# Optimization experiments

Measured on AMD Instinct MI355X. Metric: run time of the kernel, lower is better.

## Reference

```python
import jax, jax.numpy as jnp
import numpy as np

N = 50000
E = 800000
NFEAT, NHID, NCLASS = 128, 64, 16


def _spmm(row, col, w, x):
    # out[i] = sum_{e: row[e]==i} w[e] * x[col[e]]  -- sparse adj @ x
    return jax.ops.segment_sum(x[col] * w[:, None], row, num_segments=N)


def _gcn_layer(x, row, col, w, W, b):
    return _spmm(row, col, w, x @ W) + b


def setup_inputs() -> dict:
    key = jax.random.key(0)
    ks = jax.random.split(key, 16)
    glorot = lambda k, fi, fo: jax.random.uniform(k, (fi, fo), jnp.float32, -1.0, 1.0) / jnp.sqrt(fi)
    inp = {
        "x": jax.random.normal(ks[0], (N, NFEAT), jnp.float32),
        "edge_row": jax.random.randint(ks[1], (E,), 0, N, jnp.int32),
        "edge_col": jax.random.randint(ks[2], (E,), 0, N, jnp.int32),
        "edge_weight": jax.random.uniform(ks[3], (E,), jnp.float32),
        "W1": glorot(ks[4], NFEAT, NHID), "b1": jnp.zeros((NHID,), jnp.float32),
        "W2": glorot(ks[5], NHID, NHID), "b2": jnp.zeros((NHID,), jnp.float32),
        "W3": glorot(ks[6], NHID, NHID), "b3": jnp.zeros((NHID,), jnp.float32),
        "W4": glorot(ks[7], NHID, NHID), "b4": jnp.zeros((NHID,), jnp.float32),
        "W5": glorot(ks[8], NHID, NCLASS), "b5": jnp.zeros((NCLASS,), jnp.float32),
    }
    return inp


def reference(x, edge_row, edge_col, edge_weight, W1, b1, W2, b2, W3, b3, W4, b4, W5, b5):
    # Inference mode: dropout is identity.
    e1 = _gcn_layer(x, edge_row, edge_col, edge_weight, W1, b1)
    h = jax.nn.relu(e1)
    e2 = _gcn_layer(h, edge_row, edge_col, edge_weight, W2, b2)
    h = jax.nn.relu(e2)
    e3 = _gcn_layer(h, edge_row, edge_col, edge_weight, W3, b3)
    h = jax.nn.relu(e3)
    e4 = _gcn_layer(h, edge_row, edge_col, edge_weight, W4, b4)
    h = jax.nn.relu(e4)
    e5 = _gcn_layer(h, edge_row, edge_col, edge_weight, W5, b5)
    return (jax.nn.log_softmax(e5, axis=1), e1, e2, e3, e4, e5)
```

## Files before the change

kernel.cpp:

```cpp
#include <hip/hip_runtime.h>
#include <math.h>

#define NN 50000
#define NE 800000
#define NFEAT 128
#define NHID 64
#define NCLASS 16
#define NB_SCAN ((NN + 255) / 256)
#define GB ((NN + 63) / 64)
#define SGRP 4
#define ROWS_PER_SGRP ((NN + SGRP - 1) / SGRP)
#define SCHUNKS 392

__device__ inline unsigned short f2bf(float f) {
    unsigned u = __builtin_bit_cast(unsigned, f);
    u += 0x7fffu + ((u >> 16) & 1u);
    return (unsigned short)(u >> 16);
}
__device__ inline float bf2f(unsigned short h) {
    return __builtin_bit_cast(float, (unsigned)h << 16);
}
__device__ inline float pk_w(unsigned v) { return bf2f((unsigned short)(v >> 16)); }
__device__ inline int pk_c(unsigned v) { return (int)(v & 0xffffu); }


__global__ __launch_bounds__(256) void hist_rank_kernel(const int* __restrict__ erow,
                                                        int* __restrict__ deg,
                                                        unsigned* __restrict__ rr, int E) {
    int e = blockIdx.x * 256 + threadIdx.x;
    if (e < E) {
        int r = erow[e];
        int k = atomicAdd(&deg[r], 1);
        rr[e] = ((unsigned)r << 16) | (unsigned)k;
    }
}

__global__ __launch_bounds__(256) void scan_sum_kernel(const int* __restrict__ deg,
                                                       int* __restrict__ blocksum, int n) {
    __shared__ int s[256];
    const int t = threadIdx.x;
    int i = blockIdx.x * 256 + t;
    s[t] = (i < n) ? deg[i] : 0;
    __syncthreads();
#pragma unroll
    for (int off = 128; off > 0; off >>= 1) {
        if (t < off) s[t] += s[t + off];
        __syncthreads();
    }
    if (t == 0) blocksum[blockIdx.x] = s[0];
}

__global__ __launch_bounds__(256) void scan_final_kernel(const int* __restrict__ deg,
                                                         const int* __restrict__ blocksum,
                                                         int* __restrict__ row_ptr, int n) {
    __shared__ int bs[256];
    __shared__ int s[256];
    const int t = threadIdx.x;
    bs[t] = (t < NB_SCAN) ? blocksum[t] : 0;
    __syncthreads();
    for (int off = 1; off < 256; off <<= 1) {
        int u = (t >= off) ? bs[t - off] : 0;
        __syncthreads();
        bs[t] += u;
        __syncthreads();
    }
    const int blockpre = (blockIdx.x == 0) ? 0 : bs[blockIdx.x - 1];

    int i = blockIdx.x * 256 + t;
    int d = (i < n) ? deg[i] : 0;
    s[t] = d;
    __syncthreads();
    for (int off = 1; off < 256; off <<= 1) {
        int u = (t >= off) ? s[t - off] : 0;
        __syncthreads();
        s[t] += u;
        __syncthreads();
    }
    int excl = blockpre + s[t] - d;
    if (i < n) {
        row_ptr[i] = excl;
        if (i == n - 1) row_ptr[n] = excl + d;
    }
}

__global__ __launch_bounds__(256) void scatter_rank_kernel(const unsigned* __restrict__ rr,
                                                           const int* __restrict__ ecol,
                                                           const float* __restrict__ ew,
                                                           const int* __restrict__ row_ptr,
                                                           unsigned* __restrict__ pk, int E) {
    const int g = blockIdx.x & (SGRP - 1);
    const int chunk = blockIdx.x / SGRP;
    const int CH = (E + SCHUNKS - 1) / SCHUNKS;
    const int lo = chunk * CH;
    const int hi = (lo + CH < E) ? lo + CH : E;
    for (int e = lo + threadIdx.x; e < hi; e += 256) {
        unsigned v = rr[e];
        int r = (int)(v >> 16);
        if (r / ROWS_PER_SGRP == g) {
            int pos = row_ptr[r] + (int)(v & 0xffffu);
            pk[pos] = ((unsigned)f2bf(ew[e]) << 16) | (unsigned)ecol[e];
        }
    }
}

template <int K, bool RELU_IN>
__global__ __launch_bounds__(256) void gemm64_kernel(const float* __restrict__ in,
                                                     const float* __restrict__ Wg,
                                                     unsigned short* __restrict__ outb, int M) {
    constexpr int KC = 64;
    __shared__ float xs[KC][68];
    __shared__ float Ws[KC][64];
    const int t = threadIdx.x;
    const int tx = t % 16;
    const int ty = t / 16;
    const int r0 = blockIdx.x * 64;

    float acc[4][4];
#pragma unroll
    for (int i = 0; i < 4; i++)
#pragma unroll
        for (int j = 0; j < 4; j++) acc[i][j] = 0.f;

    for (int k0 = 0; k0 < K; k0 += KC) {
        for (int i = t * 4; i < KC * 64; i += 1024) {
            *(float4*)&Ws[i / 64][i % 64] = *(const float4*)&Wg[(size_t)k0 * 64 + i];
        }
        {
            const int r = t / 4;
            const int q = t % 4;
            const int gr = r0 + r;
#pragma unroll
            for (int i = 0; i < 4; i++) {
                int k = q * 16 + i * 4;
                float4 v;
                if (gr < M)
                    v = *(const float4*)&in[(size_t)gr * K + k0 + k];
                else
                    v = make_float4(0.f, 0.f, 0.f, 0.f);
                if (RELU_IN) {
                    v.x = fmaxf(v.x, 0.f);
                    v.y = fmaxf(v.y, 0.f);
                    v.z = fmaxf(v.z, 0.f);
                    v.w = fmaxf(v.w, 0.f);
                }
                xs[k + 0][r] = v.x;
                xs[k + 1][r] = v.y;
                xs[k + 2][r] = v.z;
                xs[k + 3][r] = v.w;
            }
        }
        __syncthreads();
#pragma unroll 8
        for (int k = 0; k < KC; k++) {
            float4 xv = *(const float4*)&xs[k][ty * 4];
            float4 wv = *(const float4*)&Ws[k][tx * 4];
            acc[0][0] += xv.x * wv.x; acc[0][1] += xv.x * wv.y;
            acc[0][2] += xv.x * wv.z; acc[0][3] += xv.x * wv.w;
            acc[1][0] += xv.y * wv.x; acc[1][1] += xv.y * wv.y;
            acc[1][2] += xv.y * wv.z; acc[1][3] += xv.y * wv.w;
            acc[2][0] += xv.z * wv.x; acc[2][1] += xv.z * wv.y;
            acc[2][2] += xv.z * wv.z; acc[2][3] += xv.z * wv.w;
            acc[3][0] += xv.w * wv.x; acc[3][1] += xv.w * wv.y;
            acc[3][2] += xv.w * wv.z; acc[3][3] += xv.w * wv.w;
        }
        __syncthreads();
    }
#pragma unroll
    for (int i = 0; i < 4; i++) {
        int r = r0 + ty * 4 + i;
        if (r < M) {
            ushort4 u;
            u.x = f2bf(acc[i][0]);
            u.y = f2bf(acc[i][1]);
            u.z = f2bf(acc[i][2]);
            u.w = f2bf(acc[i][3]);
            *(ushort4*)&outb[(size_t)r * 64 + tx * 4] = u;
        }
    }
}

template <int K, int NOUT, int RPT, bool RELU_IN>
__global__ __launch_bounds__(256) void gemm16_kernel(const float* __restrict__ in,
                                                     const float* __restrict__ Wg,
                                                     unsigned short* __restrict__ outb, int M) {
    __shared__ float Wl[K * NOUT];
    for (int i = threadIdx.x * 4; i < K * NOUT; i += 256 * 4) {
        *(float4*)&Wl[i] = *(const float4*)&Wg[i];
    }
    __syncthreads();

    constexpr int GROUPS = 256 / NOUT;
    constexpr int RPB = GROUPS * RPT;
    const int col = threadIdx.x % NOUT;
    const int grp = threadIdx.x / NOUT;
    const int r = blockIdx.x * RPB + grp * RPT;
    if (r >= M) return;

    float acc[RPT];
#pragma unroll
    for (int j = 0; j < RPT; j++) acc[j] = 0.f;

    const float* pr = in + (size_t)r * K;
#pragma unroll 2
    for (int k = 0; k < K; k += 4) {
        float w0 = Wl[(k + 0) * NOUT + col];
        float w1 = Wl[(k + 1) * NOUT + col];
        float w2 = Wl[(k + 2) * NOUT + col];
        float w3 = Wl[(k + 3) * NOUT + col];
#pragma unroll
        for (int j = 0; j < RPT; j++) {
            float4 xv = *(const float4*)(pr + j * K + k);
            if (RELU_IN) {
                xv.x = fmaxf(xv.x, 0.f);
                xv.y = fmaxf(xv.y, 0.f);
                xv.z = fmaxf(xv.z, 0.f);
                xv.w = fmaxf(xv.w, 0.f);
            }
            acc[j] += xv.x * w0;
            acc[j] += xv.y * w1;
            acc[j] += xv.z * w2;
            acc[j] += xv.w * w3;
        }
    }
#pragma unroll
    for (int j = 0; j < RPT; j++) {
        if (r + j < M) outb[(size_t)(r + j) * NOUT + col] = f2bf(acc[j]);
    }
}

__global__ __launch_bounds__(256) void spmm64v2_kernel(const unsigned short* __restrict__ tmpb,
                                                       const int* __restrict__ row_ptr,
                                                       const unsigned* __restrict__ pk,
                                                       const float* __restrict__ bias,
                                                       float* __restrict__ e_out, int M) {
    const int t = threadIdx.x;
    const int r = blockIdx.x * 8 + (t >> 5);
    if (r >= M) return;
    const int f2 = (t & 31) * 2;

    int e = row_ptr[r];
    const int end = row_ptr[r + 1];
    float a0 = 0.f, a1 = 0.f;
    for (; e + 7 < end; e += 8) {
        unsigned q0 = pk[e + 0], q1 = pk[e + 1], q2 = pk[e + 2], q3 = pk[e + 3];
        unsigned q4 = pk[e + 4], q5 = pk[e + 5], q6 = pk[e + 6], q7 = pk[e + 7];
        unsigned g0 = *(const unsigned*)&tmpb[(size_t)pk_c(q0) * 64 + f2];
        unsigned g1 = *(const unsigned*)&tmpb[(size_t)pk_c(q1) * 64 + f2];
        unsigned g2 = *(const unsigned*)&tmpb[(size_t)pk_c(q2) * 64 + f2];
        unsigned g3 = *(const unsigned*)&tmpb[(size_t)pk_c(q3) * 64 + f2];
        unsigned g4 = *(const unsigned*)&tmpb[(size_t)pk_c(q4) * 64 + f2];
        unsigned g5 = *(const unsigned*)&tmpb[(size_t)pk_c(q5) * 64 + f2];
        unsigned g6 = *(const unsigned*)&tmpb[(size_t)pk_c(q6) * 64 + f2];
        unsigned g7 = *(const unsigned*)&tmpb[(size_t)pk_c(q7) * 64 + f2];
        a0 += pk_w(q0) * bf2f((unsigned short)(g0 & 0xffffu));
        a1 += pk_w(q0) * bf2f((unsigned short)(g0 >> 16));
        a0 += pk_w(q1) * bf2f((unsigned short)(g1 & 0xffffu));
        a1 += pk_w(q1) * bf2f((unsigned short)(g1 >> 16));
        a0 += pk_w(q2) * bf2f((unsigned short)(g2 & 0xffffu));
        a1 += pk_w(q2) * bf2f((unsigned short)(g2 >> 16));
        a0 += pk_w(q3) * bf2f((unsigned short)(g3 & 0xffffu));
        a1 += pk_w(q3) * bf2f((unsigned short)(g3 >> 16));
        a0 += pk_w(q4) * bf2f((unsigned short)(g4 & 0xffffu));
        a1 += pk_w(q4) * bf2f((unsigned short)(g4 >> 16));
        a0 += pk_w(q5) * bf2f((unsigned short)(g5 & 0xffffu));
        a1 += pk_w(q5) * bf2f((unsigned short)(g5 >> 16));
        a0 += pk_w(q6) * bf2f((unsigned short)(g6 & 0xffffu));
        a1 += pk_w(q6) * bf2f((unsigned short)(g6 >> 16));
        a0 += pk_w(q7) * bf2f((unsigned short)(g7 & 0xffffu));
        a1 += pk_w(q7) * bf2f((unsigned short)(g7 >> 16));
    }
    for (; e < end; e++) {
        unsigned q = pk[e];
        unsigned g = *(const unsigned*)&tmpb[(size_t)pk_c(q) * 64 + f2];
        a0 += pk_w(q) * bf2f((unsigned short)(g & 0xffffu));
        a1 += pk_w(q) * bf2f((unsigned short)(g >> 16));
    }
    float2 v;
    v.x = a0 + bias[f2];
    v.y = a1 + bias[f2 + 1];
    *(float2*)&e_out[(size_t)r * 64 + f2] = v;
}

__global__ __launch_bounds__(256) void spmm16_lsm_kernel(const unsigned short* __restrict__ tmpc,
                                                         const int* __restrict__ row_ptr,
                                                         const unsigned* __restrict__ pk,
                                                         const float* __restrict__ bias,
                                                         float* __restrict__ e5,
                                                         float* __restrict__ out0, int M) {
    const int f = threadIdx.x & 15;
    const int rl = threadIdx.x >> 4;
    const int r = blockIdx.x * 16 + rl;
    if (r >= M) return;

    int e = row_ptr[r];
    const int end = row_ptr[r + 1];
    float acc = 0.f;
    for (; e + 7 < end; e += 8) {
        unsigned q0 = pk[e + 0], q1 = pk[e + 1], q2 = pk[e + 2], q3 = pk[e + 3];
        unsigned q4 = pk[e + 4], q5 = pk[e + 5], q6 = pk[e + 6], q7 = pk[e + 7];
        acc += pk_w(q0) * bf2f(tmpc[(size_t)pk_c(q0) * 16 + f]);
        acc += pk_w(q1) * bf2f(tmpc[(size_t)pk_c(q1) * 16 + f]);
        acc += pk_w(q2) * bf2f(tmpc[(size_t)pk_c(q2) * 16 + f]);
        acc += pk_w(q3) * bf2f(tmpc[(size_t)pk_c(q3) * 16 + f]);
        acc += pk_w(q4) * bf2f(tmpc[(size_t)pk_c(q4) * 16 + f]);
        acc += pk_w(q5) * bf2f(tmpc[(size_t)pk_c(q5) * 16 + f]);
        acc += pk_w(q6) * bf2f(tmpc[(size_t)pk_c(q6) * 16 + f]);
        acc += pk_w(q7) * bf2f(tmpc[(size_t)pk_c(q7) * 16 + f]);
    }
    for (; e < end; e++) {
        unsigned q = pk[e];
        acc += pk_w(q) * bf2f(tmpc[(size_t)pk_c(q) * 16 + f]);
    }
    float v = acc + bias[f];
    e5[(size_t)r * 16 + f] = v;

    float m = v;
#pragma unroll
    for (int off = 1; off < 16; off <<= 1) m = fmaxf(m, __shfl_xor(m, off, 16));
    float s = expf(v - m);
#pragma unroll
    for (int off = 1; off < 16; off <<= 1) s += __shfl_xor(s, off, 16);
    float ls = logf(s);
    out0[(size_t)r * 16 + f] = v - m - ls;
}


extern "C" void kernel_launch(void* const* d_in, const int* in_sizes, int n_in,
                              void* d_out, int out_size, void* d_ws, size_t ws_size,
                              hipStream_t stream) {
    const float* x = (const float*)d_in[0];
    const int* erow = (const int*)d_in[1];
    const int* ecol = (const int*)d_in[2];
    const float* ew = (const float*)d_in[3];
    const float* W1 = (const float*)d_in[4];
    const float* b1 = (const float*)d_in[5];
    const float* W2 = (const float*)d_in[6];
    const float* b2 = (const float*)d_in[7];
    const float* W3 = (const float*)d_in[8];
    const float* b3 = (const float*)d_in[9];
    const float* W4 = (const float*)d_in[10];
    const float* b4 = (const float*)d_in[11];
    const float* W5 = (const float*)d_in[12];
    const float* b5 = (const float*)d_in[13];

    float* out0 = (float*)d_out;
    float* e1 = out0 + (size_t)NN * NCLASS;
    float* e2 = e1 + (size_t)NN * NHID;
    float* e3 = e2 + (size_t)NN * NHID;
    float* e4 = e3 + (size_t)NN * NHID;
    float* e5 = e4 + (size_t)NN * NHID;

    char* ws = (char*)d_ws;
    unsigned short* tmpb = (unsigned short*)ws; ws += (size_t)NN * NHID * 2;
    unsigned short* tmpc = (unsigned short*)ws; ws += ((size_t)NN * NCLASS * 2 + 255) / 256 * 256;
    int* deg = (int*)ws;       ws += ((size_t)NN * 4 + 255) / 256 * 256;
    int* row_ptr = (int*)ws;   ws += ((size_t)(NN + 1) * 4 + 255) / 256 * 256;
    int* blocksum = (int*)ws;  ws += ((size_t)NB_SCAN * 4 + 255) / 256 * 256;
    unsigned* rr = (unsigned*)ws; ws += (size_t)NE * 4;
    unsigned* pk = (unsigned*)ws; ws += (size_t)NE * 4;

    hipMemsetAsync(deg, 0, (size_t)NN * 4, stream);
    hist_rank_kernel<<<(NE + 255) / 256, 256, 0, stream>>>(erow, deg, rr, NE);
    scan_sum_kernel<<<NB_SCAN, 256, 0, stream>>>(deg, blocksum, NN);
    scan_final_kernel<<<NB_SCAN, 256, 0, stream>>>(deg, blocksum, row_ptr, NN);
    scatter_rank_kernel<<<SGRP * SCHUNKS, 256, 0, stream>>>(rr, ecol, ew, row_ptr, pk, NE);

    gemm64_kernel<NFEAT, false><<<GB, 256, 0, stream>>>(x, W1, tmpb, NN);
    spmm64v2_kernel<<<(NN + 7) / 8, 256, 0, stream>>>(tmpb, row_ptr, pk, b1, e1, NN);

    gemm64_kernel<NHID, true><<<GB, 256, 0, stream>>>(e1, W2, tmpb, NN);
    spmm64v2_kernel<<<(NN + 7) / 8, 256, 0, stream>>>(tmpb, row_ptr, pk, b2, e2, NN);

    gemm64_kernel<NHID, true><<<GB, 256, 0, stream>>>(e2, W3, tmpb, NN);
    spmm64v2_kernel<<<(NN + 7) / 8, 256, 0, stream>>>(tmpb, row_ptr, pk, b3, e3, NN);

    gemm64_kernel<NHID, true><<<GB, 256, 0, stream>>>(e3, W4, tmpb, NN);
    spmm64v2_kernel<<<(NN + 7) / 8, 256, 0, stream>>>(tmpb, row_ptr, pk, b4, e4, NN);

    gemm16_kernel<NHID, NCLASS, 4, true><<<GB, 256, 0, stream>>>(e4, W5, tmpc, NN);
    spmm16_lsm_kernel<<<(NN + 15) / 16, 256, 0, stream>>>(tmpc, row_ptr, pk, b5, e5, out0, NN);
}
```

Measured before the change: 343.8 us.

## Fuse next-layer GEMM into SpMM epilogue and simplify CSR build

Each 64-wide SpMM kernel now also applies ReLU and multiplies by the next layer's weight matrix from shared memory, writing the bf16 projected features directly. This removes the separate gemm launches and the fp32 re-read of e1..e4. CSR construction switches to an atomic-cursor scatter instead of the rank-based grouped scatter, which makes edge order within a row nondeterministic. The final 16-class SpMM splits edges across four lane groups per wavefront and reduces them with shuffles.

```diff
diff --git a/kernel.cpp b/kernel.cpp
--- a/kernel.cpp
+++ b/kernel.cpp
@@ -8,9 +8,6 @@
 #define NCLASS 16
 #define NB_SCAN ((NN + 255) / 256)
 #define GB ((NN + 63) / 64)
-#define SGRP 4
-#define ROWS_PER_SGRP ((NN + SGRP - 1) / SGRP)
-#define SCHUNKS 392
 
 __device__ inline unsigned short f2bf(float f) {
     unsigned u = __builtin_bit_cast(unsigned, f);
@@ -24,15 +21,10 @@
 __device__ inline int pk_c(unsigned v) { return (int)(v & 0xffffu); }
 
 
-__global__ __launch_bounds__(256) void hist_rank_kernel(const int* __restrict__ erow,
-                                                        int* __restrict__ deg,
-                                                        unsigned* __restrict__ rr, int E) {
+__global__ __launch_bounds__(256) void hist_kernel(const int* __restrict__ erow,
+                                                   int* __restrict__ deg, int E) {
     int e = blockIdx.x * 256 + threadIdx.x;
-    if (e < E) {
-        int r = erow[e];
-        int k = atomicAdd(&deg[r], 1);
-        rr[e] = ((unsigned)r << 16) | (unsigned)k;
-    }
+    if (e < E) atomicAdd(&deg[erow[e]], 1);
 }
 
 __global__ __launch_bounds__(256) void scan_sum_kernel(const int* __restrict__ deg,
@@ -52,7 +44,8 @@
 
 __global__ __launch_bounds__(256) void scan_final_kernel(const int* __restrict__ deg,
                                                          const int* __restrict__ blocksum,
-                                                         int* __restrict__ row_ptr, int n) {
+                                                         int* __restrict__ row_ptr,
+                                                         int* __restrict__ cursor, int n) {
     __shared__ int bs[256];
     __shared__ int s[256];
     const int t = threadIdx.x;
@@ -79,27 +72,21 @@
     int excl = blockpre + s[t] - d;
     if (i < n) {
         row_ptr[i] = excl;
+        cursor[i] = excl;
         if (i == n - 1) row_ptr[n] = excl + d;
     }
 }
 
-__global__ __launch_bounds__(256) void scatter_rank_kernel(const unsigned* __restrict__ rr,
-                                                           const int* __restrict__ ecol,
-                                                           const float* __restrict__ ew,
-                                                           const int* __restrict__ row_ptr,
-                                                           unsigned* __restrict__ pk, int E) {
-    const int g = blockIdx.x & (SGRP - 1);
-    const int chunk = blockIdx.x / SGRP;
-    const int CH = (E + SCHUNKS - 1) / SCHUNKS;
-    const int lo = chunk * CH;
-    const int hi = (lo + CH < E) ? lo + CH : E;
-    for (int e = lo + threadIdx.x; e < hi; e += 256) {
-        unsigned v = rr[e];
-        int r = (int)(v >> 16);
-        if (r / ROWS_PER_SGRP == g) {
-            int pos = row_ptr[r] + (int)(v & 0xffffu);
-            pk[pos] = ((unsigned)f2bf(ew[e]) << 16) | (unsigned)ecol[e];
-        }
+__global__ __launch_bounds__(256) void scatter_atomic_kernel(const int* __restrict__ erow,
+                                                             const int* __restrict__ ecol,
+                                                             const float* __restrict__ ew,
+                                                             int* __restrict__ cursor,
+                                                             unsigned* __restrict__ pk, int E) {
+    int e = blockIdx.x * 256 + threadIdx.x;
+    if (e < E) {
+        int r = erow[e];
+        int pos = atomicAdd(&cursor[r], 1);
+        pk[pos] = ((unsigned)f2bf(ew[e]) << 16) | (unsigned)ecol[e];
     }
 }
 
@@ -179,106 +166,73 @@
     }
 }
 
-template <int K, int NOUT, int RPT, bool RELU_IN>
-__global__ __launch_bounds__(256) void gemm16_kernel(const float* __restrict__ in,
-                                                     const float* __restrict__ Wg,
-                                                     unsigned short* __restrict__ outb, int M) {
-    __shared__ float Wl[K * NOUT];
-    for (int i = threadIdx.x * 4; i < K * NOUT; i += 256 * 4) {
-        *(float4*)&Wl[i] = *(const float4*)&Wg[i];
-    }
-    __syncthreads();
-
-    constexpr int GROUPS = 256 / NOUT;
-    constexpr int RPB = GROUPS * RPT;
-    const int col = threadIdx.x % NOUT;
-    const int grp = threadIdx.x / NOUT;
-    const int r = blockIdx.x * RPB + grp * RPT;
-    if (r >= M) return;
-
-    float acc[RPT];
-#pragma unroll
-    for (int j = 0; j < RPT; j++) acc[j] = 0.f;
-
-    const float* pr = in + (size_t)r * K;
-#pragma unroll 2
-    for (int k = 0; k < K; k += 4) {
-        float w0 = Wl[(k + 0) * NOUT + col];
-        float w1 = Wl[(k + 1) * NOUT + col];
-        float w2 = Wl[(k + 2) * NOUT + col];
-        float w3 = Wl[(k + 3) * NOUT + col];
-#pragma unroll
-        for (int j = 0; j < RPT; j++) {
-            float4 xv = *(const float4*)(pr + j * K + k);
-            if (RELU_IN) {
-                xv.x = fmaxf(xv.x, 0.f);
-                xv.y = fmaxf(xv.y, 0.f);
-                xv.z = fmaxf(xv.z, 0.f);
-                xv.w = fmaxf(xv.w, 0.f);
-            }
-            acc[j] += xv.x * w0;
-            acc[j] += xv.y * w1;
-            acc[j] += xv.z * w2;
-            acc[j] += xv.w * w3;
-        }
-    }
-#pragma unroll
-    for (int j = 0; j < RPT; j++) {
-        if (r + j < M) outb[(size_t)(r + j) * NOUT + col] = f2bf(acc[j]);
-    }
-}
-
-__global__ __launch_bounds__(256) void spmm64v2_kernel(const unsigned short* __restrict__ tmpb,
-                                                       const int* __restrict__ row_ptr,
-                                                       const unsigned* __restrict__ pk,
-                                                       const float* __restrict__ bias,
-                                                       float* __restrict__ e_out, int M) {
-    const int t = threadIdx.x;
-    const int r = blockIdx.x * 8 + (t >> 5);
-    if (r >= M) return;
-    const int f2 = (t & 31) * 2;
-
+template <int NOUT>
+__global__ __launch_bounds__(512) void spmm64_fused_kernel(
+    const unsigned short* __restrict__ gb,
+    const int* __restrict__ row_ptr,
+    const unsigned* __restrict__ pk,
+    const float* __restrict__ bias,
+    const float* __restrict__ Wn,
+    float* __restrict__ e_out,
+    unsigned short* __restrict__ nxt,
+    int M) {
+    __shared__ float Wlt[NOUT][65];
+    __shared__ float xs[8][64];
+    const int t = threadIdx.x;
+
+    for (int idx = t; idx < 64 * NOUT; idx += 512) {
+        int k = idx / NOUT, j = idx % NOUT;
+        Wlt[j][k] = Wn[idx];
+    }
+
+    const int wv = __builtin_amdgcn_readfirstlane(t >> 6);
+    const int lane = t & 63;
+    int r = blockIdx.x * 8 + wv;
+    if (r >= M) r = M - 1;
+
+    float a = 0.f;
     int e = row_ptr[r];
     const int end = row_ptr[r + 1];
-    float a0 = 0.f, a1 = 0.f;
-    for (; e + 7 < end; e += 8) {
+    for (; e + 8 <= end; e += 8) {
         unsigned q0 = pk[e + 0], q1 = pk[e + 1], q2 = pk[e + 2], q3 = pk[e + 3];
         unsigned q4 = pk[e + 4], q5 = pk[e + 5], q6 = pk[e + 6], q7 = pk[e + 7];
-        unsigned g0 = *(const unsigned*)&tmpb[(size_t)pk_c(q0) * 64 + f2];
-        unsigned g1 = *(const unsigned*)&tmpb[(size_t)pk_c(q1) * 64 + f2];
-        unsigned g2 = *(const unsigned*)&tmpb[(size_t)pk_c(q2) * 64 + f2];
-        unsigned g3 = *(const unsigned*)&tmpb[(size_t)pk_c(q3) * 64 + f2];
-        unsigned g4 = *(const unsigned*)&tmpb[(size_t)pk_c(q4) * 64 + f2];
-        unsigned g5 = *(const unsigned*)&tmpb[(size_t)pk_c(q5) * 64 + f2];
-        unsigned g6 = *(const unsigned*)&tmpb[(size_t)pk_c(q6) * 64 + f2];
-        unsigned g7 = *(const unsigned*)&tmpb[(size_t)pk_c(q7) * 64 + f2];
-        a0 += pk_w(q0) * bf2f((unsigned short)(g0 & 0xffffu));
-        a1 += pk_w(q0) * bf2f((unsigned short)(g0 >> 16));
-        a0 += pk_w(q1) * bf2f((unsigned short)(g1 & 0xffffu));
-        a1 += pk_w(q1) * bf2f((unsigned short)(g1 >> 16));
-        a0 += pk_w(q2) * bf2f((unsigned short)(g2 & 0xffffu));
-        a1 += pk_w(q2) * bf2f((unsigned short)(g2 >> 16));
-        a0 += pk_w(q3) * bf2f((unsigned short)(g3 & 0xffffu));
-        a1 += pk_w(q3) * bf2f((unsigned short)(g3 >> 16));
-        a0 += pk_w(q4) * bf2f((unsigned short)(g4 & 0xffffu));
-        a1 += pk_w(q4) * bf2f((unsigned short)(g4 >> 16));
-        a0 += pk_w(q5) * bf2f((unsigned short)(g5 & 0xffffu));
-        a1 += pk_w(q5) * bf2f((unsigned short)(g5 >> 16));
-        a0 += pk_w(q6) * bf2f((unsigned short)(g6 & 0xffffu));
-        a1 += pk_w(q6) * bf2f((unsigned short)(g6 >> 16));
-        a0 += pk_w(q7) * bf2f((unsigned short)(g7 & 0xffffu));
-        a1 += pk_w(q7) * bf2f((unsigned short)(g7 >> 16));
-    }
-    for (; e < end; e++) {
+        a += pk_w(q0) * bf2f(gb[(size_t)pk_c(q0) * 64 + lane]);
+        a += pk_w(q1) * bf2f(gb[(size_t)pk_c(q1) * 64 + lane]);
+        a += pk_w(q2) * bf2f(gb[(size_t)pk_c(q2) * 64 + lane]);
+        a += pk_w(q3) * bf2f(gb[(size_t)pk_c(q3) * 64 + lane]);
+        a += pk_w(q4) * bf2f(gb[(size_t)pk_c(q4) * 64 + lane]);
+        a += pk_w(q5) * bf2f(gb[(size_t)pk_c(q5) * 64 + lane]);
+        a += pk_w(q6) * bf2f(gb[(size_t)pk_c(q6) * 64 + lane]);
+        a += pk_w(q7) * bf2f(gb[(size_t)pk_c(q7) * 64 + lane]);
+    }
+    for (; e < end; ++e) {
         unsigned q = pk[e];
-        unsigned g = *(const unsigned*)&tmpb[(size_t)pk_c(q) * 64 + f2];
-        a0 += pk_w(q) * bf2f((unsigned short)(g & 0xffffu));
-        a1 += pk_w(q) * bf2f((unsigned short)(g >> 16));
-    }
-    float2 v;
-    v.x = a0 + bias[f2];
-    v.y = a1 + bias[f2 + 1];
-    *(float2*)&e_out[(size_t)r * 64 + f2] = v;
+        a += pk_w(q) * bf2f(gb[(size_t)pk_c(q) * 64 + lane]);
+    }
+    float v = a + bias[lane];
+    e_out[(size_t)r * 64 + lane] = v;
+    xs[wv][lane] = fmaxf(v, 0.f);
+    __syncthreads();
+
+    if (NOUT == 64) {
+        const int rr = t >> 6;
+        const int j = t & 63;
+        float acc = 0.f;
+#pragma unroll 16
+        for (int k = 0; k < 64; k++) acc += xs[rr][k] * Wlt[j][k];
+        int gr = blockIdx.x * 8 + rr;
+        if (gr < M) nxt[(size_t)gr * 64 + j] = f2bf(acc);
+    } else {
+        if (t < 8 * NOUT) {
+            const int rr = t / NOUT;
+            const int j = t % NOUT;
+            float acc = 0.f;
+#pragma unroll 16
+            for (int k = 0; k < 64; k++) acc += xs[rr][k] * Wlt[j][k];
+            int gr = blockIdx.x * 8 + rr;
+            if (gr < M) nxt[(size_t)gr * NOUT + j] = f2bf(acc);
+        }
+    }
 }
 
 __global__ __launch_bounds__(256) void spmm16_lsm_kernel(const unsigned short* __restrict__ tmpc,
@@ -287,41 +241,47 @@
                                                          const float* __restrict__ bias,
                                                          float* __restrict__ e5,
                                                          float* __restrict__ out0, int M) {
-    const int f = threadIdx.x & 15;
-    const int rl = threadIdx.x >> 4;
-    const int r = blockIdx.x * 16 + rl;
+    const int t = threadIdx.x;
+    const int wv = __builtin_amdgcn_readfirstlane(t >> 6);
+    const int lane = t & 63;
+    const int f = lane & 15;
+    const int s = lane >> 4;
+    const int r = blockIdx.x * 4 + wv;
     if (r >= M) return;
 
     int e = row_ptr[r];
     const int end = row_ptr[r + 1];
     float acc = 0.f;
-    for (; e + 7 < end; e += 8) {
-        unsigned q0 = pk[e + 0], q1 = pk[e + 1], q2 = pk[e + 2], q3 = pk[e + 3];
-        unsigned q4 = pk[e + 4], q5 = pk[e + 5], q6 = pk[e + 6], q7 = pk[e + 7];
-        acc += pk_w(q0) * bf2f(tmpc[(size_t)pk_c(q0) * 16 + f]);
-        acc += pk_w(q1) * bf2f(tmpc[(size_t)pk_c(q1) * 16 + f]);
-        acc += pk_w(q2) * bf2f(tmpc[(size_t)pk_c(q2) * 16 + f]);
-        acc += pk_w(q3) * bf2f(tmpc[(size_t)pk_c(q3) * 16 + f]);
-        acc += pk_w(q4) * bf2f(tmpc[(size_t)pk_c(q4) * 16 + f]);
-        acc += pk_w(q5) * bf2f(tmpc[(size_t)pk_c(q5) * 16 + f]);
-        acc += pk_w(q6) * bf2f(tmpc[(size_t)pk_c(q6) * 16 + f]);
-        acc += pk_w(q7) * bf2f(tmpc[(size_t)pk_c(q7) * 16 + f]);
-    }
-    for (; e < end; e++) {
-        unsigned q = pk[e];
+    for (; e + 8 <= end; e += 8) {
+        unsigned qa = pk[e + s];
+        unsigned qb = pk[e + 4 + s];
+        acc += pk_w(qa) * bf2f(tmpc[(size_t)pk_c(qa) * 16 + f]);
+        acc += pk_w(qb) * bf2f(tmpc[(size_t)pk_c(qb) * 16 + f]);
+    }
+    if (e + 4 <= end) {
+        unsigned q = pk[e + s];
         acc += pk_w(q) * bf2f(tmpc[(size_t)pk_c(q) * 16 + f]);
-    }
+        e += 4;
+    }
+    if (s < end - e) {
+        unsigned q = pk[e + s];
+        acc += pk_w(q) * bf2f(tmpc[(size_t)pk_c(q) * 16 + f]);
+    }
+    acc += __shfl_xor(acc, 16);
+    acc += __shfl_xor(acc, 32);
     float v = acc + bias[f];
-    e5[(size_t)r * 16 + f] = v;
 
     float m = v;
 #pragma unroll
     for (int off = 1; off < 16; off <<= 1) m = fmaxf(m, __shfl_xor(m, off, 16));
-    float s = expf(v - m);
-#pragma unroll
-    for (int off = 1; off < 16; off <<= 1) s += __shfl_xor(s, off, 16);
-    float ls = logf(s);
-    out0[(size_t)r * 16 + f] = v - m - ls;
+    float sum = expf(v - m);
+#pragma unroll
+    for (int off = 1; off < 16; off <<= 1) sum += __shfl_xor(sum, off, 16);
+    float ls = logf(sum);
+    if (lane < 16) {
+        e5[(size_t)r * 16 + f] = v;
+        out0[(size_t)r * 16 + f] = v - m - ls;
+    }
 }
 
 
@@ -351,32 +311,28 @@
     float* e5 = e4 + (size_t)NN * NHID;
 
     char* ws = (char*)d_ws;
-    unsigned short* tmpb = (unsigned short*)ws; ws += (size_t)NN * NHID * 2;
+    unsigned short* tmpA = (unsigned short*)ws; ws += (size_t)NN * NHID * 2;
+    unsigned short* tmpB = (unsigned short*)ws; ws += (size_t)NN * NHID * 2;
     unsigned short* tmpc = (unsigned short*)ws; ws += ((size_t)NN * NCLASS * 2 + 255) / 256 * 256;
-    int* deg = (int*)ws;       ws += ((size_t)NN * 4 + 255) / 256 * 256;
-    int* row_ptr = (int*)ws;   ws += ((size_t)(NN + 1) * 4 + 255) / 256 * 256;
-    int* blocksum = (int*)ws;  ws += ((size_t)NB_SCAN * 4 + 255) / 256 * 256;
-    unsigned* rr = (unsigned*)ws; ws += (size_t)NE * 4;
+    int* deg = (int*)ws;      ws += ((size_t)NN * 4 + 255) / 256 * 256;
+    int* row_ptr = (int*)ws;  ws += ((size_t)(NN + 1) * 4 + 255) / 256 * 256;
+    int* cursor = (int*)ws;   ws += ((size_t)NN * 4 + 255) / 256 * 256;
+    int* blocksum = (int*)ws; ws += ((size_t)NB_SCAN * 4 + 255) / 256 * 256;
     unsigned* pk = (unsigned*)ws; ws += (size_t)NE * 4;
 
     hipMemsetAsync(deg, 0, (size_t)NN * 4, stream);
-    hist_rank_kernel<<<(NE + 255) / 256, 256, 0, stream>>>(erow, deg, rr, NE);
+    hist_kernel<<<(NE + 255) / 256, 256, 0, stream>>>(erow, deg, NE);
     scan_sum_kernel<<<NB_SCAN, 256, 0, stream>>>(deg, blocksum, NN);
-    scan_final_kernel<<<NB_SCAN, 256, 0, stream>>>(deg, blocksum, row_ptr, NN);
-    scatter_rank_kernel<<<SGRP * SCHUNKS, 256, 0, stream>>>(rr, ecol, ew, row_ptr, pk, NE);
-
-    gemm64_kernel<NFEAT, false><<<GB, 256, 0, stream>>>(x, W1, tmpb, NN);
-    spmm64v2_kernel<<<(NN + 7) / 8, 256, 0, stream>>>(tmpb, row_ptr, pk, b1, e1, NN);
-
-    gemm64_kernel<NHID, true><<<GB, 256, 0, stream>>>(e1, W2, tmpb, NN);
-    spmm64v2_kernel<<<(NN + 7) / 8, 256, 0, stream>>>(tmpb, row_ptr, pk, b2, e2, NN);
-
-    gemm64_kernel<NHID, true><<<GB, 256, 0, stream>>>(e2, W3, tmpb, NN);
-    spmm64v2_kernel<<<(NN + 7) / 8, 256, 0, stream>>>(tmpb, row_ptr, pk, b3, e3, NN);
-
-    gemm64_kernel<NHID, true><<<GB, 256, 0, stream>>>(e3, W4, tmpb, NN);
-    spmm64v2_kernel<<<(NN + 7) / 8, 256, 0, stream>>>(tmpb, row_ptr, pk, b4, e4, NN);
-
-    gemm16_kernel<NHID, NCLASS, 4, true><<<GB, 256, 0, stream>>>(e4, W5, tmpc, NN);
-    spmm16_lsm_kernel<<<(NN + 15) / 16, 256, 0, stream>>>(tmpc, row_ptr, pk, b5, e5, out0, NN);
-}
+    scan_final_kernel<<<NB_SCAN, 256, 0, stream>>>(deg, blocksum, row_ptr, cursor, NN);
+    scatter_atomic_kernel<<<(NE + 255) / 256, 256, 0, stream>>>(erow, ecol, ew, cursor, pk, NE);
+
+    gemm64_kernel<NFEAT, false><<<GB, 256, 0, stream>>>(x, W1, tmpA, NN);
+
+    const int FG = NN / 8;
+    spmm64_fused_kernel<64><<<FG, 512, 0, stream>>>(tmpA, row_ptr, pk, b1, W2, e1, tmpB, NN);
+    spmm64_fused_kernel<64><<<FG, 512, 0, stream>>>(tmpB, row_ptr, pk, b2, W3, e2, tmpA, NN);
+    spmm64_fused_kernel<64><<<FG, 512, 0, stream>>>(tmpA, row_ptr, pk, b3, W4, e3, tmpB, NN);
+    spmm64_fused_kernel<16><<<FG, 512, 0, stream>>>(tmpB, row_ptr, pk, b4, W5, e4, tmpc, NN);
+
+    spmm16_lsm_kernel<<<(NN + 3) / 4, 256, 0, stream>>>(tmpc, row_ptr, pk, b5, e5, out0, NN);
+}
```

Measured after the change: 381.6 us. 11.0% more time.
